# Kernel optimization log

Measured on AMD Instinct MI355X. Metric: run time of the kernel, lower is better.

Reference implementation:

```python
import jax, jax.numpy as jnp
import numpy as np

TAU = 10.0
EPS = 1e-6
TOP_K = 8


def setup_inputs() -> dict:
    key = jax.random.key(0)
    ks = jax.random.split(key, 5)
    D, NB, H = 1024, 512, 4096
    B, S = 4, 2048
    x = jax.random.normal(ks[0], (B, S, D), dtype=jnp.float32)
    W1 = jax.random.normal(ks[1], (H, D), dtype=jnp.float32) * (1.0 / np.sqrt(D))
    W2 = jax.random.normal(ks[2], (D, H), dtype=jnp.float32) * (1.0 / np.sqrt(H))
    ln_g = jnp.ones((D,), jnp.float32)
    ln_b = jnp.zeros((D,), jnp.float32)
    router_W = jax.random.normal(ks[3], (NB, D), dtype=jnp.float32) * 0.01
    router_b = jnp.zeros((NB,), jnp.float32)
    raw_U = jax.random.normal(ks[4], (NB, D), dtype=jnp.float32) * 0.02
    raw_V = jax.random.normal(jax.random.fold_in(key, 7), (NB, D), dtype=jnp.float32) * 0.02
    gamma = jnp.ones((1, 1, D), jnp.float32) * 0.1
    return {"x": x, "W1": W1, "W2": W2, "ln_g": ln_g, "ln_b": ln_b,
            "router_W": router_W, "router_b": router_b,
            "raw_U": raw_U, "raw_V": raw_V, "gamma": gamma}


def _layernorm(x, g, b):
    mu = jnp.mean(x, axis=-1, keepdims=True)
    var = jnp.var(x, axis=-1, keepdims=True)
    return (x - mu) * jax.lax.rsqrt(var + 1e-5) * g + b


def _unit_rows(W):
    n = jnp.linalg.norm(W, axis=1, keepdims=True)
    return W / jnp.maximum(n, EPS)


def reference(x, W1, W2, ln_g, ln_b, router_W, router_b, raw_U, raw_V, gamma):
    B, S, D = x.shape
    x_flat = x.reshape(-1, D)                      # [N, D]
    r_raw = _layernorm(x_flat, ln_g, ln_b) @ router_W.T + router_b  # [N, NB]
    r = jnp.clip(r_raw, -TAU, TAU)
    alpha = jax.nn.softplus(r)
    phi, idx = jax.lax.top_k(alpha, TOP_K)         # [N, K]
    S_sum = jnp.sum(phi, axis=-1, keepdims=True)
    Z = (phi / (S_sum + EPS)) * jnp.tanh(S_sum)    # [N, K]
    U_sel = _unit_rows(raw_U)[idx]                 # [N, K, D]
    V_sel = _unit_rows(raw_V)[idx]                 # [N, K, D]
    h_lat = jnp.einsum('nd,nkd->nk', x_flat, U_sel)
    dyn = jnp.einsum('nk,nkd->nd', h_lat * Z, V_sel).reshape(B, S, D) * gamma
    static = (jax.nn.gelu(x_flat @ W1.T, approximate=False) @ W2.T).reshape(B, S, D)
    return static + dyn
```

## Files before the change

### kernel.cpp

```cpp
#include <hip/hip_runtime.h>
#include <hip/hip_bf16.h>
#include <math.h>

#define N_TOK 8192
#define DDIM  1024
#define HDIM  4096
#define NBLK  512

typedef __bf16 bf16x8 __attribute__((ext_vector_type(8)));
typedef __bf16 bf16x4 __attribute__((ext_vector_type(4)));
typedef float  floatx4 __attribute__((ext_vector_type(4)));

__device__ __forceinline__ float wave_reduce_sum(float v) {
#pragma unroll
    for (int off = 32; off > 0; off >>= 1) v += __shfl_down(v, off, 64);
    return v;
}

__device__ __forceinline__ void gload_lds16(const void* g, void* l) {
    __builtin_amdgcn_global_load_lds((const __attribute__((address_space(1))) void*)g,
                                     (__attribute__((address_space(3))) void*)l,
                                     16, 0, 0);
}

__device__ __forceinline__ float fast_gelu(float x) {
    float ax = fabsf(x);
    float z  = ax * 0.70710678118654752f;
    float t  = __builtin_amdgcn_rcpf(fmaf(0.3275911f, z, 1.0f));
    float p  = fmaf(fmaf(fmaf(fmaf(1.061405429f, t, -1.453152027f),
                              t, 1.421413741f),
                         t, -0.284496736f),
                    t, 0.254829592f);
    p *= t;
    float e = __expf(-z * z);
    float E = fmaf(-p, e, 1.0f);
    return 0.5f * fmaf(ax, E, x);
}

__device__ __forceinline__ float fast_softplus(float r) {
    return __logf(fmaf(1.0f, __expf(r), 1.0f));
}

__device__ __forceinline__ void cast1024(const float* __restrict__ s,
                                         __bf16* __restrict__ d,
                                         size_t off, int t) {
    float4 v = ((const float4*)(s + off))[t];
    bf16x4 o;
    o.x = (__bf16)v.x; o.y = (__bf16)v.y;
    o.z = (__bf16)v.z; o.w = (__bf16)v.w;
    ((bf16x4*)(d + off))[t] = o;
}

__global__ __launch_bounds__(256) void prep_kernel(
        const float* __restrict__ x,
        const float* __restrict__ ln_g, const float* __restrict__ ln_b,
        const float* __restrict__ W1,   const float* __restrict__ W2,
        const float* __restrict__ router_W,
        const float* __restrict__ rawU, const float* __restrict__ rawV,
        __bf16* __restrict__ xb,  __bf16* __restrict__ lnb,
        __bf16* __restrict__ w1b, __bf16* __restrict__ w2b,
        __bf16* __restrict__ rwb,
        float* __restrict__ unitU, float* __restrict__ unitV) {
    int b = blockIdx.x;
    int t = threadIdx.x;

    if (b < 1024) {
        const float* src = (b < NBLK) ? rawU + (size_t)b * DDIM
                                      : rawV + (size_t)(b - NBLK) * DDIM;
        float* dst = (b < NBLK) ? unitU + (size_t)b * DDIM
                                : unitV + (size_t)(b - NBLK) * DDIM;
        float vals[4];
        float ss = 0.f;
#pragma unroll
        for (int i = 0; i < 4; i++) { vals[i] = src[t + i * 256]; ss += vals[i] * vals[i]; }
        __shared__ float red[4];
        ss = wave_reduce_sum(ss);
        if ((t & 63) == 0) red[t >> 6] = ss;
        __syncthreads();
        float tot = red[0] + red[1] + red[2] + red[3];
        float inv = 1.f / fmaxf(sqrtf(tot), 1e-6f);
#pragma unroll
        for (int i = 0; i < 4; i++) dst[t + i * 256] = vals[i] * inv;
    } else if (b < 9216) {
        int n = b - 1024;
        const float* row = x + (size_t)n * DDIM;
        float v[4];
        float s1 = 0.f, s2 = 0.f;
#pragma unroll
        for (int i = 0; i < 4; i++) {
            v[i] = row[t + i * 256];
            s1 += v[i];
            s2 += v[i] * v[i];
        }
        __shared__ float r1[4], r2[4];
        s1 = wave_reduce_sum(s1);
        s2 = wave_reduce_sum(s2);
        if ((t & 63) == 0) { r1[t >> 6] = s1; r2[t >> 6] = s2; }
        __syncthreads();
        float mu  = (r1[0] + r1[1] + r1[2] + r1[3]) * (1.f / DDIM);
        float var = (r2[0] + r2[1] + r2[2] + r2[3]) * (1.f / DDIM) - mu * mu;
        float rstd = rsqrtf(var + 1e-5f);
        __bf16* orow = lnb + (size_t)n * DDIM;
        __bf16* xrow = xb  + (size_t)n * DDIM;
#pragma unroll
        for (int i = 0; i < 4; i++) {
            int d = t + i * 256;
            orow[d] = (__bf16)((v[i] - mu) * rstd * ln_g[d] + ln_b[d]);
            xrow[d] = (__bf16)v[i];
        }
    } else if (b < 13312) {
        cast1024(W1, w1b, (size_t)(b - 9216) * 1024, t);
    } else if (b < 17408) {
        cast1024(W2, w2b, (size_t)(b - 13312) * 1024, t);
    } else {
        cast1024(router_W, rwb, (size_t)(b - 17408) * 1024, t);
    }
}

template <int MODE>
__global__ __launch_bounds__(256) void mfma_gemm(const __bf16* __restrict__ A,
                                                 const __bf16* __restrict__ B,
                                                 const float* __restrict__ bias,
                                                 void* __restrict__ Cv,
                                                 int M, int Nn, int Kk) {
    __shared__ __align__(16) __bf16 As[128 * 32];
    __shared__ __align__(16) __bf16 Bs[128 * 32];

    const int t    = threadIdx.x;
    const int lane = t & 63;
    const int wave = t >> 6;
    const int wm   = wave >> 1, wn = wave & 1;
    const int lr   = lane & 15, quad = lane >> 4;
    const int m0   = blockIdx.x * 128;
    const int n0   = blockIdx.y * 128;

    const int ma0 = t >> 2,         ca0 = t & 3;
    const int ma1 = (256 + t) >> 2;
    const __bf16* Ag0 = A + (size_t)(m0 + ma0) * Kk + ca0 * 8;
    const __bf16* Ag1 = A + (size_t)(m0 + ma1) * Kk + ca0 * 8;
    const __bf16* Bg0 = B + (size_t)(n0 + ma0) * Kk + ca0 * 8;
    const __bf16* Bg1 = B + (size_t)(n0 + ma1) * Kk + ca0 * 8;
    __bf16* ldsA0 = As + t * 8;
    __bf16* ldsA1 = As + (256 + t) * 8;
    __bf16* ldsB0 = Bs + t * 8;
    __bf16* ldsB1 = Bs + (256 + t) * 8;

    const __bf16* ra[4];
    const __bf16* rb[4];
#pragma unroll
    for (int i = 0; i < 4; i++) {
        ra[i] = As + (wm * 64 + i * 16 + lr) * 32 + quad * 8;
        rb[i] = Bs + (wn * 64 + i * 16 + lr) * 32 + quad * 8;
    }

    floatx4 acc[4][4];
#pragma unroll
    for (int i = 0; i < 4; i++)
#pragma unroll
        for (int j = 0; j < 4; j++) acc[i][j] = (floatx4)0.f;

    for (int k0 = 0; k0 < Kk; k0 += 32) {
        gload_lds16(Ag0 + k0, ldsA0);
        gload_lds16(Ag1 + k0, ldsA1);
        gload_lds16(Bg0 + k0, ldsB0);
        gload_lds16(Bg1 + k0, ldsB1);
        __syncthreads();

        bf16x8 af[4], bfr[4];
#pragma unroll
        for (int i = 0; i < 4; i++) af[i]  = *(const bf16x8*)ra[i];
#pragma unroll
        for (int j = 0; j < 4; j++) bfr[j] = *(const bf16x8*)rb[j];
#pragma unroll
        for (int i = 0; i < 4; i++)
#pragma unroll
            for (int j = 0; j < 4; j++)
                acc[i][j] = __builtin_amdgcn_mfma_f32_16x16x32_bf16(af[i], bfr[j],
                                                                    acc[i][j], 0, 0, 0);
        __syncthreads();
    }

    const int mBase = m0 + wm * 64 + quad * 4;
    const int nBase = n0 + wn * 64 + lr;
#pragma unroll
    for (int i = 0; i < 4; i++) {
#pragma unroll
        for (int j = 0; j < 4; j++) {
            int n = nBase + j * 16;
#pragma unroll
            for (int r = 0; r < 4; r++) {
                int m = mBase + i * 16 + r;
                float v = acc[i][j][r];
                if (MODE == 0) {
                    float rr = v + bias[n];
                    rr = fminf(fmaxf(rr, -10.f), 10.f);
                    ((float*)Cv)[(size_t)m * Nn + n] = fast_softplus(rr);
                } else if (MODE == 1) {
                    ((__bf16*)Cv)[(size_t)m * Nn + n] = (__bf16)fast_gelu(v);
                } else {
                    ((float*)Cv)[(size_t)m * Nn + n] += v;
                }
            }
        }
    }
}

__global__ __launch_bounds__(256) void topk_dyn_kernel(
        const float* __restrict__ alpha,
        const float* __restrict__ x,
        const float* __restrict__ unitU,
        const float* __restrict__ unitV,
        const float* __restrict__ gamma,
        float* __restrict__ out) {
    int n = blockIdx.x;
    int t = threadIdx.x;
    int lane = t & 63, wid = t >> 6;

    __shared__ int   sidx[8];
    __shared__ float shz[8];
    __shared__ float red[8][4];
    __shared__ float hz[8];

    if (wid == 0) {
        const float* row = alpha + (size_t)n * NBLK;
        float v[8];
#pragma unroll
        for (int i = 0; i < 8; i++) v[i] = row[lane + i * 64];
        float topv[8];
        int   topi[8];
        for (int s = 0; s < 8; s++) {
            float bv = v[0]; int bi = 0;
#pragma unroll
            for (int i = 1; i < 8; i++)
                if (v[i] > bv) { bv = v[i]; bi = i; }
            int gidx = lane + bi * 64;
#pragma unroll
            for (int off = 1; off < 64; off <<= 1) {
                float ov = __shfl_xor(bv, off, 64);
                int   oi = __shfl_xor(gidx, off, 64);
                if (ov > bv || (ov == bv && oi < gidx)) { bv = ov; gidx = oi; }
            }
            topv[s] = bv; topi[s] = gidx;
            if ((gidx & 63) == lane) v[gidx >> 6] = -1e30f;
        }
        float S = 0.f;
#pragma unroll
        for (int s = 0; s < 8; s++) S += topv[s];
        float zscale = tanhf(S) / (S + 1e-6f);
        if (lane < 8) {
            sidx[lane] = topi[lane];
            shz[lane]  = topv[lane] * zscale;
        }
    }
    __syncthreads();

    const float* xr = x + (size_t)n * DDIM;
    float xv[4];
#pragma unroll
    for (int i = 0; i < 4; i++) xv[i] = xr[t + i * 256];

    float acc[8];
#pragma unroll
    for (int k = 0; k < 8; k++) {
        const float* ur = unitU + (size_t)sidx[k] * DDIM;
        float a = 0.f;
#pragma unroll
        for (int i = 0; i < 4; i++) a = fmaf(xv[i], ur[t + i * 256], a);
        acc[k] = a;
    }
#pragma unroll
    for (int k = 0; k < 8; k++) {
        float a = wave_reduce_sum(acc[k]);
        if (lane == 0) red[k][wid] = a;
    }
    __syncthreads();
    if (t < 8) {
        float h = red[t][0] + red[t][1] + red[t][2] + red[t][3];
        hz[t] = h * shz[t];
    }
    __syncthreads();

    float* orow = out + (size_t)n * DDIM;
#pragma unroll
    for (int i = 0; i < 4; i++) {
        int d = t + i * 256;
        float s = 0.f;
#pragma unroll
        for (int k = 0; k < 8; k++)
            s = fmaf(hz[k], unitV[(size_t)sidx[k] * DDIM + d], s);
        orow[d] = s * gamma[d];
    }
}

extern "C" void kernel_launch(void* const* d_in, const int* in_sizes, int n_in,
                              void* d_out, int out_size, void* d_ws, size_t ws_size,
                              hipStream_t stream) {
    const float* x        = (const float*)d_in[0];
    const float* W1       = (const float*)d_in[1];
    const float* W2       = (const float*)d_in[2];
    const float* ln_g     = (const float*)d_in[3];
    const float* ln_b     = (const float*)d_in[4];
    const float* router_W = (const float*)d_in[5];
    const float* router_b = (const float*)d_in[6];
    const float* raw_U    = (const float*)d_in[7];
    const float* raw_V    = (const float*)d_in[8];
    const float* gamma    = (const float*)d_in[9];
    float* out = (float*)d_out;

    char* ws = (char*)d_ws;
    __bf16* lnb   = (__bf16*)(ws);
    float*  alpha = (float*)(ws + 16777216u);
    __bf16* g1    = (__bf16*)(ws);
    __bf16* xb    = (__bf16*)(ws + 67108864u);
    __bf16* w1b   = (__bf16*)(ws + 83886080u);
    __bf16* w2b   = (__bf16*)(ws + 92274688u);
    __bf16* rwb   = (__bf16*)(ws + 100663296u);
    float*  unitU = (float*)(ws + 101711872u);
    float*  unitV = (float*)(ws + 103809024u);

    prep_kernel<<<17920, 256, 0, stream>>>(x, ln_g, ln_b, W1, W2, router_W,
                                           raw_U, raw_V, xb, lnb, w1b, w2b, rwb,
                                           unitU, unitV);

    dim3 gR(N_TOK / 128, NBLK / 128);
    mfma_gemm<0><<<gR, 256, 0, stream>>>(lnb, rwb, router_b, (void*)alpha, N_TOK, NBLK, DDIM);

    topk_dyn_kernel<<<N_TOK, 256, 0, stream>>>(alpha, x, unitU, unitV, gamma, out);

    dim3 g1d(N_TOK / 128, HDIM / 128);
    mfma_gemm<1><<<g1d, 256, 0, stream>>>(xb, w1b, nullptr, (void*)g1, N_TOK, HDIM, DDIM);

    dim3 g2d(N_TOK / 128, DDIM / 128);
    mfma_gemm<2><<<g2d, 256, 0, stream>>>(g1, w2b, nullptr, (void*)out, N_TOK, DDIM, HDIM);
}
```

Baseline: 405.8 us.

## Double-buffer LDS tiles in MFMA GEMM to overlap loads with compute

Splits the A and B shared-memory tiles into two buffers. The next K-slice is prefetched with global_load_lds into the idle buffer while MFMAs run on the current one, and the loop drops from two barriers per iteration to one. This aims to hide global-memory latency behind matrix math in all GEMM modes. It doubles LDS use per block, to 32KB, which may reduce occupancy.

```diff
diff --git a/kernel.cpp b/kernel.cpp
--- a/kernel.cpp
+++ b/kernel.cpp
@@ -123,8 +123,8 @@
                                                  const float* __restrict__ bias,
                                                  void* __restrict__ Cv,
                                                  int M, int Nn, int Kk) {
-    __shared__ __align__(16) __bf16 As[128 * 32];
-    __shared__ __align__(16) __bf16 Bs[128 * 32];
+    __shared__ __align__(16) __bf16 As[2][128 * 32];
+    __shared__ __align__(16) __bf16 Bs[2][128 * 32];
 
     const int t    = threadIdx.x;
     const int lane = t & 63;
@@ -134,23 +134,23 @@
     const int m0   = blockIdx.x * 128;
     const int n0   = blockIdx.y * 128;
 
-    const int ma0 = t >> 2,         ca0 = t & 3;
-    const int ma1 = (256 + t) >> 2;
-    const __bf16* Ag0 = A + (size_t)(m0 + ma0) * Kk + ca0 * 8;
-    const __bf16* Ag1 = A + (size_t)(m0 + ma1) * Kk + ca0 * 8;
-    const __bf16* Bg0 = B + (size_t)(n0 + ma0) * Kk + ca0 * 8;
-    const __bf16* Bg1 = B + (size_t)(n0 + ma1) * Kk + ca0 * 8;
-    __bf16* ldsA0 = As + t * 8;
-    __bf16* ldsA1 = As + (256 + t) * 8;
-    __bf16* ldsB0 = Bs + t * 8;
-    __bf16* ldsB1 = Bs + (256 + t) * 8;
-
-    const __bf16* ra[4];
-    const __bf16* rb[4];
+    const int ca0 = t & 3;
+    const __bf16* Ag[2];
+    const __bf16* Bg[2];
+    int ldsOff[2];
+#pragma unroll
+    for (int q = 0; q < 2; q++) {
+        int idx = q * 256 + t;
+        Ag[q]     = A + (size_t)(m0 + (idx >> 2)) * Kk + ca0 * 8;
+        Bg[q]     = B + (size_t)(n0 + (idx >> 2)) * Kk + ca0 * 8;
+        ldsOff[q] = idx * 8;
+    }
+
+    int raOff[4], rbOff[4];
 #pragma unroll
     for (int i = 0; i < 4; i++) {
-        ra[i] = As + (wm * 64 + i * 16 + lr) * 32 + quad * 8;
-        rb[i] = Bs + (wn * 64 + i * 16 + lr) * 32 + quad * 8;
+        raOff[i] = (wm * 64 + i * 16 + lr) * 32 + quad * 8;
+        rbOff[i] = (wn * 64 + i * 16 + lr) * 32 + quad * 8;
     }
 
     floatx4 acc[4][4];
@@ -159,25 +159,36 @@
 #pragma unroll
         for (int j = 0; j < 4; j++) acc[i][j] = (floatx4)0.f;
 
-    for (int k0 = 0; k0 < Kk; k0 += 32) {
-        gload_lds16(Ag0 + k0, ldsA0);
-        gload_lds16(Ag1 + k0, ldsA1);
-        gload_lds16(Bg0 + k0, ldsB0);
-        gload_lds16(Bg1 + k0, ldsB1);
+#pragma unroll
+    for (int q = 0; q < 2; q++) {
+        gload_lds16(Ag[q], &As[0][ldsOff[q]]);
+        gload_lds16(Bg[q], &Bs[0][ldsOff[q]]);
+    }
+
+    const int niter = Kk >> 5;
+    for (int it = 0; it < niter; ++it) {
+        const int cur = it & 1;
         __syncthreads();
-
+        if (it + 1 < niter) {
+            const int nk = (it + 1) << 5;
+            const int nb = cur ^ 1;
+#pragma unroll
+            for (int q = 0; q < 2; q++) {
+                gload_lds16(Ag[q] + nk, &As[nb][ldsOff[q]]);
+                gload_lds16(Bg[q] + nk, &Bs[nb][ldsOff[q]]);
+            }
+        }
         bf16x8 af[4], bfr[4];
 #pragma unroll
-        for (int i = 0; i < 4; i++) af[i]  = *(const bf16x8*)ra[i];
-#pragma unroll
-        for (int j = 0; j < 4; j++) bfr[j] = *(const bf16x8*)rb[j];
+        for (int i = 0; i < 4; i++) af[i]  = *(const bf16x8*)&As[cur][raOff[i]];
+#pragma unroll
+        for (int j = 0; j < 4; j++) bfr[j] = *(const bf16x8*)&Bs[cur][rbOff[j]];
 #pragma unroll
         for (int i = 0; i < 4; i++)
 #pragma unroll
             for (int j = 0; j < 4; j++)
                 acc[i][j] = __builtin_amdgcn_mfma_f32_16x16x32_bf16(af[i], bfr[j],
                                                                     acc[i][j], 0, 0, 0);
-        __syncthreads();
     }
 
     const int mBase = m0 + wm * 64 + quad * 4;
```

After: 385.4 us. 5.0% less time.
